# Optimization experiments

Measured on AMD Instinct MI355X. Metric: run time of the kernel, lower is better.

## Reference

```python
import jax, jax.numpy as jnp
import numpy as np

B, I, O, K = 4096, 1024, 1024, 16

def setup_inputs() -> dict:
    key = jax.random.key(0)
    k1, k2 = jax.random.split(key)
    x = jax.random.normal(k1, (B, I), dtype=jnp.float32)
    weights = jax.random.normal(k2, (O, I, K), dtype=jnp.float32)
    bias = jnp.zeros((O,), dtype=jnp.float32)
    centers = jnp.linspace(-1.0, 1.0, K, dtype=jnp.float32)
    widths = jnp.full((K,), 0.1, dtype=jnp.float32)
    return {"x": x, "weights": weights, "bias": bias, "centers": centers, "widths": widths}

def reference(x, weights, bias, centers, widths):
    # Gaussian RBF basis: [B, I, K]
    diff = x[:, :, None] - centers[None, None, :]
    kernels = jnp.exp(-(diff ** 2) / (2.0 * widths[None, None, :] ** 2))
    # Contraction over input_dim and num_kernels (GEMM-equivalent)
    out = jnp.einsum('bik,oik->bo', kernels, weights)
    return out + bias
```

## Files before the change

### kernel.cpp

```cpp
#include <hip/hip_runtime.h>
#include <hip/hip_bf16.h>


#define B_DIM 4096
#define I_DIM 1024
#define O_DIM 1024
#define NK 16
#define KD (I_DIM * NK)

typedef unsigned short u16;
typedef __attribute__((ext_vector_type(8))) __bf16 bf16x8;
typedef __attribute__((ext_vector_type(4))) float f32x4;
typedef __attribute__((ext_vector_type(8))) unsigned short u16x8;

typedef const __attribute__((address_space(1))) unsigned short gu16;
typedef __attribute__((address_space(3))) unsigned short lu16;

static __device__ __forceinline__ u16 f2bf(float f) {
  unsigned u = __float_as_uint(f);
  u += 0x7FFFu + ((u >> 16) & 1u);
  return (u16)(u >> 16);
}

__global__ void __launch_bounds__(256) rbf_feat(const float* __restrict__ x,
                                                u16* __restrict__ feat,
                                                const float* __restrict__ centers,
                                                const float* __restrict__ widths) {
  const int idx = blockIdx.x * 256 + threadIdx.x;
  const float xv = x[idx];
  u16x8 lo, hi;
#pragma unroll
  for (int k = 0; k < 16; ++k) {
    const float c = centers[k];
    const float w = widths[k];
    const float s = -0.5f * __builtin_amdgcn_rcpf(w * w);
    const float d = xv - c;
    const u16 h = f2bf(__expf(d * d * s));
    if (k < 8) lo[k] = h; else hi[k - 8] = h;
  }
  u16x8* dst = (u16x8*)(feat + (size_t)idx * 16);
  dst[0] = lo;
  dst[1] = hi;
}

__global__ void __launch_bounds__(256) cvt_w(const float4* __restrict__ w,
                                             u16x8* __restrict__ wb) {
  const size_t i = (size_t)blockIdx.x * 256 + threadIdx.x;
  const float4 a = w[2 * i];
  const float4 b = w[2 * i + 1];
  u16x8 o;
  o[0] = f2bf(a.x); o[1] = f2bf(a.y); o[2] = f2bf(a.z); o[3] = f2bf(a.w);
  o[4] = f2bf(b.x); o[5] = f2bf(b.y); o[6] = f2bf(b.z); o[7] = f2bf(b.w);
  wb[i] = o;
}

static __device__ __forceinline__ void stage_half(const u16* __restrict__ g,
                                                  u16* __restrict__ lds, int t) {
#pragma unroll
  for (int j = 0; j < 2; ++j) {
    const int chunk = j * 512 + t;
    const int row = chunk >> 3, slot = chunk & 7;
    const int c = slot ^ (row & 7);
    __builtin_amdgcn_global_load_lds((gu16*)(g + (size_t)row * KD + c * 8),
                                     (lu16*)(lds + chunk * 8), 16, 0, 0);
  }
}

#define NT 64

__global__ void __launch_bounds__(512, 2)
gemm8(const u16* __restrict__ A, const u16* __restrict__ Bm,
      float* __restrict__ part) {
  __shared__ u16 sA[2][2][128 * 64];
  __shared__ u16 sB[2][2][128 * 64];

  const int t = threadIdx.x;
  const int bm = blockIdx.x;
  const int bn = blockIdx.y;
  const int kz = blockIdx.z;
  const int wid = t >> 6, l = t & 63;
  const int wr = wid >> 2, wc = wid & 3;
  const int lm = l & 15, lk = l >> 4;

  const u16* aT = A + (size_t)(bm * 256) * KD + kz * 4096;
  const u16* bT = Bm + (size_t)(bn * 256) * KD + kz * 4096;

  const int swz0 = ((0 * 4 + lk) ^ (lm & 7)) * 8;
  const int swz1 = ((1 * 4 + lk) ^ (lm & 7)) * 8;
  const int arow = wr * 64 + lm;
  const int brow = wc * 32 + lm;

  f32x4 acc[8][4];
#pragma unroll
  for (int i = 0; i < 8; ++i)
#pragma unroll
    for (int j = 0; j < 4; ++j)
      acc[i][j] = (f32x4){0.f, 0.f, 0.f, 0.f};

  stage_half(aT, &sA[0][0][0], t);
  stage_half(aT + (size_t)128 * KD, &sA[0][1][0], t);
  stage_half(bT, &sB[0][0][0], t);
  stage_half(bT + (size_t)128 * KD, &sB[0][1][0], t);
  stage_half(bT + 64, &sB[1][0][0], t);
  stage_half(aT + 64, &sA[1][0][0], t);
  asm volatile("s_waitcnt vmcnt(4)" ::: "memory");
  __builtin_amdgcn_s_barrier();

  for (int T = 0; T < NT; ++T) {
    const int c = T & 1;

    bf16x8 aq[4][2], b0[2][2], b1[2][2];
#pragma unroll
    for (int mi = 0; mi < 4; ++mi) {
      aq[mi][0] = *(const bf16x8*)&sA[c][0][(arow + mi * 16) * 64 + swz0];
      aq[mi][1] = *(const bf16x8*)&sA[c][0][(arow + mi * 16) * 64 + swz1];
    }
#pragma unroll
    for (int ni = 0; ni < 2; ++ni) {
      b0[ni][0] = *(const bf16x8*)&sB[c][0][(brow + ni * 16) * 64 + swz0];
      b0[ni][1] = *(const bf16x8*)&sB[c][0][(brow + ni * 16) * 64 + swz1];
      b1[ni][0] = *(const bf16x8*)&sB[c][1][(brow + ni * 16) * 64 + swz0];
      b1[ni][1] = *(const bf16x8*)&sB[c][1][(brow + ni * 16) * 64 + swz1];
    }
    if (T + 1 < NT) {
      stage_half(aT + (size_t)128 * KD + (T + 1) * 64, &sA[(T + 1) & 1][1][0], t);
      stage_half(bT + (size_t)128 * KD + (T + 1) * 64, &sB[(T + 1) & 1][1][0], t);
    }

    __builtin_amdgcn_s_setprio(1);
#pragma unroll
    for (int mi = 0; mi < 4; ++mi)
#pragma unroll
      for (int ni = 0; ni < 2; ++ni)
#pragma unroll
        for (int kk = 0; kk < 2; ++kk)
          acc[mi][ni] = __builtin_amdgcn_mfma_f32_16x16x32_bf16(
              aq[mi][kk], b0[ni][kk], acc[mi][ni], 0, 0, 0);
#pragma unroll
    for (int mi = 0; mi < 4; ++mi)
#pragma unroll
      for (int ni = 0; ni < 2; ++ni)
#pragma unroll
        for (int kk = 0; kk < 2; ++kk)
          acc[mi][2 + ni] = __builtin_amdgcn_mfma_f32_16x16x32_bf16(
              aq[mi][kk], b1[ni][kk], acc[mi][2 + ni], 0, 0, 0);
    __builtin_amdgcn_s_setprio(0);

    asm volatile("s_waitcnt lgkmcnt(0)" ::: "memory");
    __builtin_amdgcn_sched_barrier(0);
    __builtin_amdgcn_s_barrier();

    bf16x8 aq2[4][2];
#pragma unroll
    for (int mi = 0; mi < 4; ++mi) {
      aq2[mi][0] = *(const bf16x8*)&sA[c][1][(arow + mi * 16) * 64 + swz0];
      aq2[mi][1] = *(const bf16x8*)&sA[c][1][(arow + mi * 16) * 64 + swz1];
    }
    if (T + 2 < NT) {
      stage_half(bT + (T + 2) * 64, &sB[T & 1][0][0], t);
      stage_half(aT + (T + 2) * 64, &sA[T & 1][0][0], t);
    }

    __builtin_amdgcn_s_setprio(1);
#pragma unroll
    for (int mi = 0; mi < 4; ++mi)
#pragma unroll
      for (int ni = 0; ni < 2; ++ni)
#pragma unroll
        for (int kk = 0; kk < 2; ++kk)
          acc[4 + mi][2 + ni] = __builtin_amdgcn_mfma_f32_16x16x32_bf16(
              aq2[mi][kk], b1[ni][kk], acc[4 + mi][2 + ni], 0, 0, 0);
#pragma unroll
    for (int mi = 0; mi < 4; ++mi)
#pragma unroll
      for (int ni = 0; ni < 2; ++ni)
#pragma unroll
        for (int kk = 0; kk < 2; ++kk)
          acc[4 + mi][ni] = __builtin_amdgcn_mfma_f32_16x16x32_bf16(
              aq2[mi][kk], b0[ni][kk], acc[4 + mi][ni], 0, 0, 0);
    __builtin_amdgcn_s_setprio(0);

    if (T + 2 < NT) asm volatile("s_waitcnt vmcnt(4)" ::: "memory");
    else            asm volatile("s_waitcnt vmcnt(0)" ::: "memory");
    __builtin_amdgcn_s_barrier();
  }

  float* pW = part + (size_t)kz * ((size_t)B_DIM * O_DIM);
#pragma unroll
  for (int qa = 0; qa < 2; ++qa)
#pragma unroll
    for (int mi = 0; mi < 4; ++mi)
#pragma unroll
      for (int qb = 0; qb < 2; ++qb)
#pragma unroll
        for (int ni = 0; ni < 2; ++ni) {
          const int row0 = bm * 256 + qa * 128 + wr * 64 + mi * 16 + lk * 4;
          const int col = bn * 256 + qb * 128 + wc * 32 + ni * 16 + lm;
#pragma unroll
          for (int j = 0; j < 4; ++j)
            pW[(size_t)(row0 + j) * O_DIM + col] = acc[qa * 4 + mi][qb * 2 + ni][j];
        }
}

__global__ void __launch_bounds__(256) reduce4(const float4* __restrict__ p,
                                               const float4* __restrict__ bias4,
                                               float4* __restrict__ out) {
  const int i = blockIdx.x * 256 + threadIdx.x;
  const size_t s = (size_t)B_DIM * O_DIM / 4;
  const float4 a = p[i], b = p[i + s], c = p[i + 2 * s], d = p[i + 3 * s];
  const float4 bb = bias4[i & 255];
  float4 r;
  r.x = a.x + b.x + c.x + d.x + bb.x;
  r.y = a.y + b.y + c.y + d.y + bb.y;
  r.z = a.z + b.z + c.z + d.z + bb.z;
  r.w = a.w + b.w + c.w + d.w + bb.w;
  out[i] = r;
}

#define BM 128
#define BN 64
#define BK 64

__global__ void __launch_bounds__(256, 2) gemm_bt(const u16* __restrict__ A,
                                                  const u16* __restrict__ Bm,
                                                  const float* __restrict__ bias,
                                                  float* __restrict__ C) {
  __shared__ u16 sA[BM * BK];
  __shared__ u16 sB[BN * BK];

  const int t = threadIdx.x;
  const int bm = blockIdx.x, bn = blockIdx.y;
  const int wid = t >> 6, l = t & 63;
  const int wr = wid >> 1, wc = wid & 1;
  const int lm = l & 15, lk = l >> 4;

  const u16* aG = A + (size_t)bm * BM * KD;
  const u16* bG = Bm + (size_t)bn * BN * KD;

  f32x4 acc[4][2];
#pragma unroll
  for (int mi = 0; mi < 4; ++mi)
#pragma unroll
    for (int ni = 0; ni < 2; ++ni)
      acc[mi][ni] = (f32x4){0.f, 0.f, 0.f, 0.f};

  for (int kt = 0; kt < KD; kt += BK) {
#pragma unroll
    for (int j = 0; j < 4; ++j) {
      const int chunk = j * 256 + t;
      const int row = chunk >> 3, slot = chunk & 7;
      const int c = slot ^ (row & 7);
      __builtin_amdgcn_global_load_lds((gu16*)(aG + (size_t)row * KD + kt + c * 8),
                                       (lu16*)(sA + chunk * 8), 16, 0, 0);
    }
#pragma unroll
    for (int j = 0; j < 2; ++j) {
      const int chunk = j * 256 + t;
      const int row = chunk >> 3, slot = chunk & 7;
      const int c = slot ^ (row & 7);
      __builtin_amdgcn_global_load_lds((gu16*)(bG + (size_t)row * KD + kt + c * 8),
                                       (lu16*)(sB + chunk * 8), 16, 0, 0);
    }
    __syncthreads();
#pragma unroll
    for (int kk = 0; kk < 2; ++kk) {
      const int s = (kk * 4 + lk) ^ (lm & 7);
      bf16x8 af[4], bfr[2];
#pragma unroll
      for (int mi = 0; mi < 4; ++mi)
        af[mi] = *(const bf16x8*)(sA + (wr * 64 + mi * 16 + lm) * BK + s * 8);
#pragma unroll
      for (int ni = 0; ni < 2; ++ni)
        bfr[ni] = *(const bf16x8*)(sB + (wc * 32 + ni * 16 + lm) * BK + s * 8);
#pragma unroll
      for (int mi = 0; mi < 4; ++mi)
#pragma unroll
        for (int ni = 0; ni < 2; ++ni)
          acc[mi][ni] = __builtin_amdgcn_mfma_f32_16x16x32_bf16(af[mi], bfr[ni],
                                                                acc[mi][ni], 0, 0, 0);
    }
    __syncthreads();
  }

#pragma unroll
  for (int ni = 0; ni < 2; ++ni) {
    const int col = bn * BN + wc * 32 + ni * 16 + lm;
    const float bv = bias[col];
#pragma unroll
    for (int mi = 0; mi < 4; ++mi) {
      const int row0 = bm * BM + wr * 64 + mi * 16 + lk * 4;
#pragma unroll
      for (int j = 0; j < 4; ++j)
        C[(size_t)(row0 + j) * O_DIM + col] = acc[mi][ni][j] + bv;
    }
  }
}

extern "C" void kernel_launch(void* const* d_in, const int* in_sizes, int n_in,
                              void* d_out, int out_size, void* d_ws, size_t ws_size,
                              hipStream_t stream) {
  const float* x = (const float*)d_in[0];
  const float* w = (const float*)d_in[1];
  const float* bias = (const float*)d_in[2];
  const float* centers = (const float*)d_in[3];
  const float* widths = (const float*)d_in[4];
  float* out = (float*)d_out;

  u16* feat = (u16*)d_ws;
  u16* wb = (u16*)((char*)d_ws + (size_t)B_DIM * KD * 2);
  float* part = (float*)((char*)d_ws + (size_t)B_DIM * KD * 2 + (size_t)O_DIM * KD * 2);

  rbf_feat<<<(B_DIM * I_DIM) / 256, 256, 0, stream>>>(x, feat, centers, widths);
  cvt_w<<<(O_DIM * KD) / (256 * 8), 256, 0, stream>>>((const float4*)w, (u16x8*)wb);

  const size_t need = (size_t)B_DIM * KD * 2 + (size_t)O_DIM * KD * 2 +
                      4ull * B_DIM * O_DIM * 4;
  if (ws_size >= need) {
    dim3 grid(B_DIM / 256, O_DIM / 256, 4);
    gemm8<<<grid, 512, 0, stream>>>(feat, wb, part);
    reduce4<<<(B_DIM * O_DIM / 4) / 256, 256, 0, stream>>>(
        (const float4*)part, (const float4*)bias, (float4*)out);
  } else {
    dim3 grid(B_DIM / BM, O_DIM / BN);
    gemm_bt<<<grid, 256, 0, stream>>>(feat, wb, bias, out);
  }
}
```

Baseline: 182.1 us.

## Fuse RBF feature generation into split-K GEMM A-tile staging

The separate rbf_feat kernel, which wrote a 128MB bf16 feature matrix to workspace, is removed. The GEMM now loads raw x values, computes the 16 Gaussian basis values per input in registers and writes them swizzled into LDS for the next tile, so the big feature write and re-read disappear. The cost is exp and bf16 conversion work inside the main loop, which adds VALU pressure and registers and may interfere with MFMA issue. The x loads per tile are strided 4-byte loads, and the same features are recomputed across the 4 bn blocks.

```diff
diff --git a/kernel.cpp b/kernel.cpp
--- a/kernel.cpp
+++ b/kernel.cpp
@@ -69,8 +69,9 @@
 #define NT 64
 
 __global__ void __launch_bounds__(512, 2)
-gemm8(const u16* __restrict__ A, const u16* __restrict__ Bm,
-      float* __restrict__ part) {
+gemm8(const float* __restrict__ x, const u16* __restrict__ Bm,
+      float* __restrict__ part,
+      const float* __restrict__ centers, const float* __restrict__ widths) {
   __shared__ u16 sA[2][2][128 * 64];
   __shared__ u16 sB[2][2][128 * 64];
 
@@ -82,7 +83,6 @@
   const int wr = wid >> 2, wc = wid & 3;
   const int lm = l & 15, lk = l >> 4;
 
-  const u16* aT = A + (size_t)(bm * 256) * KD + kz * 4096;
   const u16* bT = Bm + (size_t)(bn * 256) * KD + kz * 4096;
 
   const int swz0 = ((0 * 4 + lk) ^ (lm & 7)) * 8;
@@ -90,6 +90,20 @@
   const int arow = wr * 64 + lm;
   const int brow = wc * 32 + lm;
 
+  float ck[16], sk[16];
+#pragma unroll
+  for (int k = 0; k < 16; ++k) {
+    ck[k] = centers[k];
+    const float w = widths[k];
+    sk[k] = -0.5f * __builtin_amdgcn_rcpf(w * w);
+  }
+  const int ar = t >> 2;
+  const int il = t & 3;
+  const int sl0 = (il * 2) ^ (ar & 7);
+  const int sl1 = (il * 2 + 1) ^ (ar & 7);
+  const float* xlo_p = x + (size_t)(bm * 256 + ar) * I_DIM + kz * 256 + il;
+  const float* xhi_p = xlo_p + (size_t)128 * I_DIM;
+
   f32x4 acc[8][4];
 #pragma unroll
   for (int i = 0; i < 8; ++i)
@@ -97,18 +111,38 @@
     for (int j = 0; j < 4; ++j)
       acc[i][j] = (f32x4){0.f, 0.f, 0.f, 0.f};
 
-  stage_half(aT, &sA[0][0][0], t);
-  stage_half(aT + (size_t)128 * KD, &sA[0][1][0], t);
+  float xlo = xlo_p[0];
+  float xhi = xhi_p[0];
   stage_half(bT, &sB[0][0][0], t);
   stage_half(bT + (size_t)128 * KD, &sB[0][1][0], t);
   stage_half(bT + 64, &sB[1][0][0], t);
-  stage_half(aT + 64, &sA[1][0][0], t);
-  asm volatile("s_waitcnt vmcnt(4)" ::: "memory");
+  {
+    u16x8 plo, phi, qlo, qhi;
+#pragma unroll
+    for (int k = 0; k < 16; ++k) {
+      const float d0 = xlo - ck[k];
+      const u16 h0 = f2bf(__expf(d0 * d0 * sk[k]));
+      const float d1 = xhi - ck[k];
+      const u16 h1 = f2bf(__expf(d1 * d1 * sk[k]));
+      if (k < 8) { plo[k] = h0; qlo[k] = h1; }
+      else       { phi[k - 8] = h0; qhi[k - 8] = h1; }
+    }
+    *(u16x8*)&sA[0][0][ar * 64 + sl0 * 8] = plo;
+    *(u16x8*)&sA[0][0][ar * 64 + sl1 * 8] = phi;
+    *(u16x8*)&sA[0][1][ar * 64 + sl0 * 8] = qlo;
+    *(u16x8*)&sA[0][1][ar * 64 + sl1 * 8] = qhi;
+  }
+  asm volatile("s_waitcnt vmcnt(2) lgkmcnt(0)" ::: "memory");
   __builtin_amdgcn_s_barrier();
 
   for (int T = 0; T < NT; ++T) {
     const int c = T & 1;
 
+    if (T + 1 < NT) {
+      xlo = xlo_p[(T + 1) * 4];
+      xhi = xhi_p[(T + 1) * 4];
+      stage_half(bT + (size_t)128 * KD + (T + 1) * 64, &sB[(T + 1) & 1][1][0], t);
+    }
     bf16x8 aq[4][2], b0[2][2], b1[2][2];
 #pragma unroll
     for (int mi = 0; mi < 4; ++mi) {
@@ -122,10 +156,6 @@
       b1[ni][0] = *(const bf16x8*)&sB[c][1][(brow + ni * 16) * 64 + swz0];
       b1[ni][1] = *(const bf16x8*)&sB[c][1][(brow + ni * 16) * 64 + swz1];
     }
-    if (T + 1 < NT) {
-      stage_half(aT + (size_t)128 * KD + (T + 1) * 64, &sA[(T + 1) & 1][1][0], t);
-      stage_half(bT + (size_t)128 * KD + (T + 1) * 64, &sB[(T + 1) & 1][1][0], t);
-    }
 
     __builtin_amdgcn_s_setprio(1);
 #pragma unroll
@@ -150,16 +180,31 @@
     __builtin_amdgcn_sched_barrier(0);
     __builtin_amdgcn_s_barrier();
 
+    if (T + 1 < NT) {
+      u16x8 plo, phi, qlo, qhi;
+#pragma unroll
+      for (int k = 0; k < 16; ++k) {
+        const float d0 = xlo - ck[k];
+        const u16 h0 = f2bf(__expf(d0 * d0 * sk[k]));
+        const float d1 = xhi - ck[k];
+        const u16 h1 = f2bf(__expf(d1 * d1 * sk[k]));
+        if (k < 8) { plo[k] = h0; qlo[k] = h1; }
+        else       { phi[k - 8] = h0; qhi[k - 8] = h1; }
+      }
+      *(u16x8*)&sA[c ^ 1][0][ar * 64 + sl0 * 8] = plo;
+      *(u16x8*)&sA[c ^ 1][0][ar * 64 + sl1 * 8] = phi;
+      *(u16x8*)&sA[c ^ 1][1][ar * 64 + sl0 * 8] = qlo;
+      *(u16x8*)&sA[c ^ 1][1][ar * 64 + sl1 * 8] = qhi;
+    }
+
     bf16x8 aq2[4][2];
 #pragma unroll
     for (int mi = 0; mi < 4; ++mi) {
       aq2[mi][0] = *(const bf16x8*)&sA[c][1][(arow + mi * 16) * 64 + swz0];
       aq2[mi][1] = *(const bf16x8*)&sA[c][1][(arow + mi * 16) * 64 + swz1];
     }
-    if (T + 2 < NT) {
+    if (T + 2 < NT)
       stage_half(bT + (T + 2) * 64, &sB[T & 1][0][0], t);
-      stage_half(aT + (T + 2) * 64, &sA[T & 1][0][0], t);
-    }
 
     __builtin_amdgcn_s_setprio(1);
 #pragma unroll
@@ -180,8 +225,8 @@
               aq2[mi][kk], b0[ni][kk], acc[4 + mi][ni], 0, 0, 0);
     __builtin_amdgcn_s_setprio(0);
 
-    if (T + 2 < NT) asm volatile("s_waitcnt vmcnt(4)" ::: "memory");
-    else            asm volatile("s_waitcnt vmcnt(0)" ::: "memory");
+    if (T + 2 < NT) asm volatile("s_waitcnt vmcnt(2) lgkmcnt(0)" ::: "memory");
+    else            asm volatile("s_waitcnt vmcnt(0) lgkmcnt(0)" ::: "memory");
     __builtin_amdgcn_s_barrier();
   }
 
@@ -306,21 +351,23 @@
   const float* widths = (const float*)d_in[4];
   float* out = (float*)d_out;
 
-  u16* feat = (u16*)d_ws;
-  u16* wb = (u16*)((char*)d_ws + (size_t)B_DIM * KD * 2);
-  float* part = (float*)((char*)d_ws + (size_t)B_DIM * KD * 2 + (size_t)O_DIM * KD * 2);
-
-  rbf_feat<<<(B_DIM * I_DIM) / 256, 256, 0, stream>>>(x, feat, centers, widths);
-  cvt_w<<<(O_DIM * KD) / (256 * 8), 256, 0, stream>>>((const float4*)w, (u16x8*)wb);
-
-  const size_t need = (size_t)B_DIM * KD * 2 + (size_t)O_DIM * KD * 2 +
-                      4ull * B_DIM * O_DIM * 4;
-  if (ws_size >= need) {
+  const size_t wb_bytes = (size_t)O_DIM * KD * 2;
+  const size_t part_bytes = 4ull * B_DIM * O_DIM * 4;
+  const size_t need_fused = wb_bytes + part_bytes;
+
+  if (ws_size >= need_fused) {
+    u16* wb = (u16*)d_ws;
+    float* part = (float*)((char*)d_ws + wb_bytes);
+    cvt_w<<<(O_DIM * KD) / (256 * 8), 256, 0, stream>>>((const float4*)w, (u16x8*)wb);
     dim3 grid(B_DIM / 256, O_DIM / 256, 4);
-    gemm8<<<grid, 512, 0, stream>>>(feat, wb, part);
+    gemm8<<<grid, 512, 0, stream>>>(x, wb, part, centers, widths);
     reduce4<<<(B_DIM * O_DIM / 4) / 256, 256, 0, stream>>>(
         (const float4*)part, (const float4*)bias, (float4*)out);
   } else {
+    u16* feat = (u16*)d_ws;
+    u16* wb = (u16*)((char*)d_ws + (size_t)B_DIM * KD * 2);
+    rbf_feat<<<(B_DIM * I_DIM) / 256, 256, 0, stream>>>(x, feat, centers, widths);
+    cvt_w<<<(O_DIM * KD) / (256 * 8), 256, 0, stream>>>((const float4*)w, (u16x8*)wb);
     dim3 grid(B_DIM / BM, O_DIM / BN);
     gemm_bt<<<grid, 256, 0, stream>>>(feat, wb, bias, out);
   }
```

After: 203.1 us. 11.5% more time.
